# Kernel tuning notes

Hardware: AMD Instinct MI355X
Metric: run time of the kernel (lower is better)

## Reference

```python
import jax, jax.numpy as jnp
import numpy as np

N = 50000   # nodes
E = 800000  # edges (avg degree 16)
D = 128     # feature dim (in_feats and all hidden_feats)
L = 3       # number of SAGEConv layers


def setup_inputs() -> dict:
    key = jax.random.key(0)
    ks = jax.random.split(key, 3 + 3 * L)
    node_feats = jax.random.normal(ks[0], (N, D), dtype=jnp.float32)
    src = jax.random.randint(ks[1], (E,), 0, N)
    dst = jax.random.randint(ks[2], (E,), 0, N)
    inp = {"node_feats": node_feats, "src": src, "dst": dst}
    scale = 1.0 / np.sqrt(D)
    for i in range(L):
        inp[f"W_self{i}"] = (jax.random.normal(ks[3 + 3 * i], (D, D), dtype=jnp.float32) * scale)
        inp[f"W_neigh{i}"] = (jax.random.normal(ks[4 + 3 * i], (D, D), dtype=jnp.float32) * scale)
        inp[f"b{i}"] = jnp.zeros((D,), dtype=jnp.float32)
    return inp


def _sage_stack(node_feats, src, dst, layers):
    n = node_feats.shape[0]
    # in-degree per destination node, clamped so isolated nodes yield 0 aggregate
    deg = jax.ops.segment_sum(jnp.ones((src.shape[0],), dtype=node_feats.dtype), dst, num_segments=n)
    inv_deg = (1.0 / jnp.maximum(deg, 1.0))[:, None]  # [N,1]
    h = node_feats
    for (W_s, W_n, b) in layers:
        # gather neighbor feats along edges, mean-reduce into dst nodes
        agg = jax.ops.segment_sum(h[src], dst, num_segments=n) * inv_deg  # [N,D]
        # DGL SAGEConv ('mean'): fc_self(h_dst) + fc_neigh(mean_neigh) + bias, then activation
        h = jax.nn.relu(h @ W_s.T + agg @ W_n.T + b)
    return h


def reference(node_feats, src, dst, W_self0, W_neigh0, b0, W_self1, W_neigh1, b1, W_self2, W_neigh2, b2):
    layers = ((W_self0, W_neigh0, b0), (W_self1, W_neigh1, b1), (W_self2, W_neigh2, b2))
    return _sage_stack(node_feats, src, dst, layers)
```

## Files before the change

### kernel.cpp

```cpp
#include <hip/hip_runtime.h>
#include <hip/hip_bf16.h>

#define NN 50000
#define NE 800000
#define DF 128
#define NSL 128
#define SLN 391
#define CAP 8192
#define ECHUNK 1563

typedef __bf16 bf16x8 __attribute__((ext_vector_type(8)));
typedef float f32x4 __attribute__((ext_vector_type(4)));

__device__ __forceinline__ unsigned short f32_to_bf16_rne(float f) {
    unsigned int u = __float_as_uint(f);
    u += 0x7fffu + ((u >> 16) & 1u);
    return (unsigned short)(u >> 16);
}

__device__ __forceinline__ unsigned int pack_bf16x2(float lo, float hi) {
    return (unsigned int)f32_to_bf16_rne(lo) | ((unsigned int)f32_to_bf16_rne(hi) << 16);
}

__global__ void k_zero(int* __restrict__ p, int n) {
    int i = threadIdx.x;
    if (i < n) p[i] = 0;
}

__global__ __launch_bounds__(256) void k_bucket(const int* __restrict__ src, const int* __restrict__ dst,
                                                int* __restrict__ gcur, uint2* __restrict__ bucket) {
    __shared__ int cnt[NSL];
    __shared__ int rb[NSL];
    int t = threadIdx.x;
    for (int j = t; j < NSL; j += 256) cnt[j] = 0;
    __syncthreads();
    int base = blockIdx.x * ECHUNK;
    int end = base + ECHUNK;
    if (end > NE) end = NE;
    for (int i = base + t; i < end; i += 256) atomicAdd(&cnt[dst[i] / SLN], 1);
    __syncthreads();
    for (int j = t; j < NSL; j += 256) rb[j] = atomicAdd(&gcur[j], cnt[j]);
    __syncthreads();
    for (int j = t; j < NSL; j += 256) cnt[j] = rb[j];
    __syncthreads();
    for (int i = base + t; i < end; i += 256) {
        int d = dst[i];
        int s = d / SLN;
        int pos = atomicAdd(&cnt[s], 1);
        bucket[s * CAP + pos] = make_uint2((unsigned)src[i], (unsigned)d);
    }
}

__global__ void k_sbase(const int* __restrict__ gcur, int* __restrict__ sbase, int* __restrict__ row_ptr) {
    if (threadIdx.x == 0) {
        int acc = 0;
        for (int s = 0; s < NSL; ++s) {
            sbase[s] = acc;
            acc += gcur[s];
        }
        row_ptr[NN] = acc;
    }
}

__global__ __launch_bounds__(256) void k_cslice(const uint2* __restrict__ bucket, const int* __restrict__ gcur,
                                                const int* __restrict__ sbase, int* __restrict__ col,
                                                int* __restrict__ row_ptr, float* __restrict__ inv_deg) {
    __shared__ int sdeg[512];
    __shared__ int scur[512];
    int s = blockIdx.x;
    int t = threadIdx.x;
    int nbase = s * SLN;
    int ncnt = NN - nbase;
    if (ncnt > SLN) ncnt = SLN;
    int ecnt = gcur[s];
    int eb = s * CAP;
    int cb = sbase[s];
    sdeg[t] = 0;
    sdeg[t + 256] = 0;
    __syncthreads();
    for (int e = t; e < ecnt; e += 256) atomicAdd(&sdeg[bucket[eb + e].y - nbase], 1);
    __syncthreads();
    int d0 = sdeg[t], d1 = sdeg[t + 256];
    for (int off = 1; off < 512; off <<= 1) {
        int v0 = (t >= off) ? sdeg[t - off] : 0;
        int v1 = (t + 256 >= off) ? sdeg[t + 256 - off] : 0;
        __syncthreads();
        sdeg[t] += v0;
        sdeg[t + 256] += v1;
        __syncthreads();
    }
    int e0 = sdeg[t] - d0, e1 = sdeg[t + 256] - d1;
    scur[t] = e0;
    scur[t + 256] = e1;
    if (t < ncnt) {
        row_ptr[nbase + t] = cb + e0;
        inv_deg[nbase + t] = 1.0f / (float)(d0 > 1 ? d0 : 1);
    }
    if (t + 256 < ncnt) {
        row_ptr[nbase + t + 256] = cb + e1;
        inv_deg[nbase + t + 256] = 1.0f / (float)(d1 > 1 ? d1 : 1);
    }
    __syncthreads();
    for (int e = t; e < ecnt; e += 256) {
        uint2 pr = bucket[eb + e];
        int p = atomicAdd(&scur[pr.y - nbase], 1);
        col[cb + p] = (int)pr.x;
    }
}

__global__ __launch_bounds__(256) void k_f2b_all(const float* __restrict__ feats,
                                                 const float* __restrict__ w0, const float* __restrict__ w1,
                                                 const float* __restrict__ w2, const float* __restrict__ w3,
                                                 const float* __restrict__ w4, const float* __restrict__ w5,
                                                 unsigned short* __restrict__ h_bf,
                                                 unsigned short* __restrict__ Wb) {
    int i = (blockIdx.x * 256 + threadIdx.x) * 4;
    const float* fsrc;
    unsigned short* dstp;
    if (i < NN * DF) {
        fsrc = feats + i;
        dstp = h_bf + i;
    } else {
        int j = i - NN * DF;
        if (j >= 6 * DF * DF) return;
        int w = j >> 14;
        int o = j & 16383;
        const float* ws[6] = {w0, w1, w2, w3, w4, w5};
        fsrc = ws[w] + o;
        dstp = Wb + w * DF * DF + o;
    }
    float4 v = *reinterpret_cast<const float4*>(fsrc);
    ushort4 r;
    r.x = f32_to_bf16_rne(v.x);
    r.y = f32_to_bf16_rne(v.y);
    r.z = f32_to_bf16_rne(v.z);
    r.w = f32_to_bf16_rne(v.w);
    *reinterpret_cast<ushort4*>(dstp) = r;
}

__global__ __launch_bounds__(256) void k_agg(const unsigned short* __restrict__ H,
                                             const int* __restrict__ row_ptr, const int* __restrict__ col,
                                             const float* __restrict__ inv_deg,
                                             unsigned short* __restrict__ Agg, int n) {
    int wid = threadIdx.x >> 6;
    int lane = threadIdx.x & 63;
    int node = blockIdx.x * 4 + wid;
    if (node >= n) return;
    int s = row_ptr[node], e = row_ptr[node + 1];
    int g = lane >> 4;
    int l = lane & 15;
    int off = l * 8;

    float a[8];
#pragma unroll
    for (int k = 0; k < 8; ++k) a[k] = 0.f;

    for (int base = s; base < e; base += 64) {
        int rem = e - base;
        if (rem > 64) rem = 64;
        int cl = (lane < rem) ? col[base + lane] : 0;
        for (int jj = 0; jj < rem; jj += 16) {
#pragma unroll
            for (int u = 0; u < 4; ++u) {
                int idx = jj + 4 * u + g;
                int c = __shfl(cl, idx, 64);
                if (idx < rem) {
                    uint4 v = *reinterpret_cast<const uint4*>(H + (size_t)c * DF + off);
                    a[0] += __uint_as_float(v.x << 16);
                    a[1] += __uint_as_float(v.x & 0xffff0000u);
                    a[2] += __uint_as_float(v.y << 16);
                    a[3] += __uint_as_float(v.y & 0xffff0000u);
                    a[4] += __uint_as_float(v.z << 16);
                    a[5] += __uint_as_float(v.z & 0xffff0000u);
                    a[6] += __uint_as_float(v.w << 16);
                    a[7] += __uint_as_float(v.w & 0xffff0000u);
                }
            }
        }
    }

#pragma unroll
    for (int k = 0; k < 8; ++k) {
        a[k] += __shfl_xor(a[k], 16, 64);
        a[k] += __shfl_xor(a[k], 32, 64);
    }

    if (g == 0) {
        float iv = inv_deg[node];
        uint4 r;
        r.x = pack_bf16x2(a[0] * iv, a[1] * iv);
        r.y = pack_bf16x2(a[2] * iv, a[3] * iv);
        r.z = pack_bf16x2(a[4] * iv, a[5] * iv);
        r.w = pack_bf16x2(a[6] * iv, a[7] * iv);
        *reinterpret_cast<uint4*>(Agg + (size_t)node * DF + off) = r;
    }
}

__global__ __launch_bounds__(256) void k_gemm(const unsigned short* __restrict__ Hb,
                                              const unsigned short* __restrict__ Ab,
                                              const unsigned short* __restrict__ Wb,
                                              const float* __restrict__ bias,
                                              unsigned short* __restrict__ Hout,
                                              float* __restrict__ Fout,
                                              int n) {
    int brow = blockIdx.x * 64;
    int lane = threadIdx.x & 63;
    int wid = threadIdx.x >> 6;
    int l15 = lane & 15;
    int lk = (lane >> 4) * 8;
    int colb = wid * 32;

    f32x4 zero = {0.f, 0.f, 0.f, 0.f};
    f32x4 acc[4][2];
#pragma unroll
    for (int m = 0; m < 4; ++m) {
        acc[m][0] = zero;
        acc[m][1] = zero;
    }

#pragma unroll
    for (int ph = 0; ph < 2; ++ph) {
        const unsigned short* Ap = ph ? Ab : Hb;
        const unsigned short* Wp = Wb + ph * (DF * DF);
#pragma unroll
        for (int ks = 0; ks < 4; ++ks) {
            int kb = ks * 32 + lk;
            bf16x8 bfr0 = *reinterpret_cast<const bf16x8*>(Wp + (colb + l15) * DF + kb);
            bf16x8 bfr1 = *reinterpret_cast<const bf16x8*>(Wp + (colb + 16 + l15) * DF + kb);
#pragma unroll
            for (int m = 0; m < 4; ++m) {
                int r = brow + m * 16 + l15;
                if (r >= n) r = n - 1;
                bf16x8 afr = *reinterpret_cast<const bf16x8*>(Ap + (size_t)r * DF + kb);
                acc[m][0] = __builtin_amdgcn_mfma_f32_16x16x32_bf16(afr, bfr0, acc[m][0], 0, 0, 0);
                acc[m][1] = __builtin_amdgcn_mfma_f32_16x16x32_bf16(afr, bfr1, acc[m][1], 0, 0, 0);
            }
        }
    }

    __syncthreads();

    int rb = (lane >> 4) * 4;
#pragma unroll
    for (int q = 0; q < 2; ++q) {
        int o = colb + q * 16 + l15;
        float bv = bias[o];
#pragma unroll
        for (int m = 0; m < 4; ++m) {
#pragma unroll
            for (int j = 0; j < 4; ++j) {
                int r = brow + m * 16 + rb + j;
                if (r < n) {
                    float v = fmaxf(acc[m][q][j] + bv, 0.f);
                    if (Fout) Fout[(size_t)r * DF + o] = v;
                    else Hout[(size_t)r * DF + o] = f32_to_bf16_rne(v);
                }
            }
        }
    }
}

extern "C" void kernel_launch(void* const* d_in, const int* in_sizes, int n_in,
                              void* d_out, int out_size, void* d_ws, size_t ws_size,
                              hipStream_t stream) {
    const float* feats = (const float*)d_in[0];
    const int* src = (const int*)d_in[1];
    const int* dst = (const int*)d_in[2];
    const float* bias[3] = {(const float*)d_in[5], (const float*)d_in[8], (const float*)d_in[11]};

    char* ws = (char*)d_ws;
    unsigned short* h_bf = (unsigned short*)(ws);
    unsigned short* agg_bf = (unsigned short*)(ws + 12800000);
    uint2* bucket = (uint2*)(ws + 12800000);
    unsigned short* Wb = (unsigned short*)(ws + 25600000);
    int* row_ptr = (int*)(ws + 25796608);
    float* inv_deg = (float*)(ws + 25996616);
    int* col = (int*)(ws + 26196616);
    int* gcur = (int*)(ws + 29396616);
    int* sbase = (int*)(ws + 29397128);

    k_zero<<<1, 128, 0, stream>>>(gcur, NSL);
    k_bucket<<<512, 256, 0, stream>>>(src, dst, gcur, bucket);
    k_sbase<<<1, 64, 0, stream>>>(gcur, sbase, row_ptr);
    k_cslice<<<NSL, 256, 0, stream>>>(bucket, gcur, sbase, col, row_ptr, inv_deg);

    int qtot = (NN * DF + 6 * DF * DF) / 4;
    k_f2b_all<<<(qtot + 255) / 256, 256, 0, stream>>>(
        feats, (const float*)d_in[3], (const float*)d_in[4], (const float*)d_in[6],
        (const float*)d_in[7], (const float*)d_in[9], (const float*)d_in[10], h_bf, Wb);

    int gblk = (NN + 63) / 64;
    for (int l = 0; l < 3; ++l) {
        k_agg<<<(NN + 3) / 4, 256, 0, stream>>>(h_bf, row_ptr, col, inv_deg, agg_bf, NN);
        const unsigned short* Wl = Wb + l * 2 * DF * DF;
        if (l < 2)
            k_gemm<<<gblk, 256, 0, stream>>>(h_bf, agg_bf, Wl, bias[l], h_bf, nullptr, NN);
        else
            k_gemm<<<gblk, 256, 0, stream>>>(h_bf, agg_bf, Wl, bias[l], nullptr, (float*)d_out, NN);
    }
}
```

Baseline: 240.0 us.

## Overlap self-GEMM with neighbor aggregation in one interleaved kernel

The self-projection GEMM (h @ W_self + bias) moves into the aggregation kernel as every 17th block, so its MFMA work runs alongside the memory-bound gather. The result is stored as an fp32 temporary that the neighbor GEMM kernel reads back and adds before the ReLU. The separate single-thread prefix-sum kernel is also removed: each k_cslice block now sums the preceding slice counts itself. The cost is an extra fp32 N×D write and read per layer in exchange for one fewer GEMM phase in the critical path.

```diff
diff --git a/kernel.cpp b/kernel.cpp
--- a/kernel.cpp
+++ b/kernel.cpp
@@ -8,6 +8,8 @@
 #define SLN 391
 #define CAP 8192
 #define ECHUNK 1563
+#define GEMMB 782
+#define KA_GRID 13294
 
 typedef __bf16 bf16x8 __attribute__((ext_vector_type(8)));
 typedef float f32x4 __attribute__((ext_vector_type(4)));
@@ -51,22 +53,12 @@
     }
 }
 
-__global__ void k_sbase(const int* __restrict__ gcur, int* __restrict__ sbase, int* __restrict__ row_ptr) {
-    if (threadIdx.x == 0) {
-        int acc = 0;
-        for (int s = 0; s < NSL; ++s) {
-            sbase[s] = acc;
-            acc += gcur[s];
-        }
-        row_ptr[NN] = acc;
-    }
-}
-
 __global__ __launch_bounds__(256) void k_cslice(const uint2* __restrict__ bucket, const int* __restrict__ gcur,
-                                                const int* __restrict__ sbase, int* __restrict__ col,
-                                                int* __restrict__ row_ptr, float* __restrict__ inv_deg) {
+                                                int* __restrict__ col, int* __restrict__ row_ptr,
+                                                float* __restrict__ inv_deg) {
     __shared__ int sdeg[512];
     __shared__ int scur[512];
+    __shared__ int shcb;
     int s = blockIdx.x;
     int t = threadIdx.x;
     int nbase = s * SLN;
@@ -74,10 +66,16 @@
     if (ncnt > SLN) ncnt = SLN;
     int ecnt = gcur[s];
     int eb = s * CAP;
-    int cb = sbase[s];
+    if (t == 0) {
+        int acc = 0;
+        for (int i = 0; i < s; ++i) acc += gcur[i];
+        shcb = acc;
+        if (s == NSL - 1) row_ptr[NN] = acc + ecnt;
+    }
     sdeg[t] = 0;
     sdeg[t + 256] = 0;
     __syncthreads();
+    int cb = shcb;
     for (int e = t; e < ecnt; e += 256) atomicAdd(&sdeg[bucket[eb + e].y - nbase], 1);
     __syncthreads();
     int d0 = sdeg[t], d1 = sdeg[t + 256];
@@ -138,71 +136,121 @@
     *reinterpret_cast<ushort4*>(dstp) = r;
 }
 
-__global__ __launch_bounds__(256) void k_agg(const unsigned short* __restrict__ H,
-                                             const int* __restrict__ row_ptr, const int* __restrict__ col,
-                                             const float* __restrict__ inv_deg,
-                                             unsigned short* __restrict__ Agg, int n) {
+__global__ __launch_bounds__(256) void k_aggself(const unsigned short* __restrict__ H,
+                                                 const int* __restrict__ row_ptr, const int* __restrict__ col,
+                                                 const float* __restrict__ inv_deg,
+                                                 const unsigned short* __restrict__ Ws,
+                                                 const float* __restrict__ bias,
+                                                 unsigned short* __restrict__ Agg,
+                                                 float* __restrict__ Tmp, int n) {
+    int bid = blockIdx.x;
     int wid = threadIdx.x >> 6;
     int lane = threadIdx.x & 63;
-    int node = blockIdx.x * 4 + wid;
-    if (node >= n) return;
-    int s = row_ptr[node], e = row_ptr[node + 1];
     int g = lane >> 4;
     int l = lane & 15;
-    int off = l * 8;
-
-    float a[8];
-#pragma unroll
-    for (int k = 0; k < 8; ++k) a[k] = 0.f;
-
-    for (int base = s; base < e; base += 64) {
-        int rem = e - base;
-        if (rem > 64) rem = 64;
-        int cl = (lane < rem) ? col[base + lane] : 0;
-        for (int jj = 0; jj < rem; jj += 16) {
-#pragma unroll
-            for (int u = 0; u < 4; ++u) {
-                int idx = jj + 4 * u + g;
-                int c = __shfl(cl, idx, 64);
-                if (idx < rem) {
-                    uint4 v = *reinterpret_cast<const uint4*>(H + (size_t)c * DF + off);
-                    a[0] += __uint_as_float(v.x << 16);
-                    a[1] += __uint_as_float(v.x & 0xffff0000u);
-                    a[2] += __uint_as_float(v.y << 16);
-                    a[3] += __uint_as_float(v.y & 0xffff0000u);
-                    a[4] += __uint_as_float(v.z << 16);
-                    a[5] += __uint_as_float(v.z & 0xffff0000u);
-                    a[6] += __uint_as_float(v.w << 16);
-                    a[7] += __uint_as_float(v.w & 0xffff0000u);
+
+    if (bid % 17 != 0) {
+        int agg_id = (bid / 17) * 16 + (bid % 17) - 1;
+        int node = agg_id * 4 + wid;
+        if (node >= n) return;
+        int s = row_ptr[node], e = row_ptr[node + 1];
+        int off = l * 8;
+
+        float a[8];
+#pragma unroll
+        for (int k = 0; k < 8; ++k) a[k] = 0.f;
+
+        for (int base = s; base < e; base += 64) {
+            int rem = e - base;
+            if (rem > 64) rem = 64;
+            int cl = (lane < rem) ? col[base + lane] : 0;
+            for (int jj = 0; jj < rem; jj += 16) {
+#pragma unroll
+                for (int u = 0; u < 4; ++u) {
+                    int idx = jj + 4 * u + g;
+                    int c = __shfl(cl, idx, 64);
+                    if (idx < rem) {
+                        uint4 v = *reinterpret_cast<const uint4*>(H + (size_t)c * DF + off);
+                        a[0] += __uint_as_float(v.x << 16);
+                        a[1] += __uint_as_float(v.x & 0xffff0000u);
+                        a[2] += __uint_as_float(v.y << 16);
+                        a[3] += __uint_as_float(v.y & 0xffff0000u);
+                        a[4] += __uint_as_float(v.z << 16);
+                        a[5] += __uint_as_float(v.z & 0xffff0000u);
+                        a[6] += __uint_as_float(v.w << 16);
+                        a[7] += __uint_as_float(v.w & 0xffff0000u);
+                    }
                 }
             }
         }
-    }
-
-#pragma unroll
-    for (int k = 0; k < 8; ++k) {
-        a[k] += __shfl_xor(a[k], 16, 64);
-        a[k] += __shfl_xor(a[k], 32, 64);
-    }
-
-    if (g == 0) {
-        float iv = inv_deg[node];
-        uint4 r;
-        r.x = pack_bf16x2(a[0] * iv, a[1] * iv);
-        r.y = pack_bf16x2(a[2] * iv, a[3] * iv);
-        r.z = pack_bf16x2(a[4] * iv, a[5] * iv);
-        r.w = pack_bf16x2(a[6] * iv, a[7] * iv);
-        *reinterpret_cast<uint4*>(Agg + (size_t)node * DF + off) = r;
-    }
-}
-
-__global__ __launch_bounds__(256) void k_gemm(const unsigned short* __restrict__ Hb,
-                                              const unsigned short* __restrict__ Ab,
-                                              const unsigned short* __restrict__ Wb,
-                                              const float* __restrict__ bias,
-                                              unsigned short* __restrict__ Hout,
-                                              float* __restrict__ Fout,
-                                              int n) {
+
+#pragma unroll
+        for (int k = 0; k < 8; ++k) {
+            a[k] += __shfl_xor(a[k], 16, 64);
+            a[k] += __shfl_xor(a[k], 32, 64);
+        }
+
+        if (g == 0) {
+            float iv = inv_deg[node];
+            uint4 r;
+            r.x = pack_bf16x2(a[0] * iv, a[1] * iv);
+            r.y = pack_bf16x2(a[2] * iv, a[3] * iv);
+            r.z = pack_bf16x2(a[4] * iv, a[5] * iv);
+            r.w = pack_bf16x2(a[6] * iv, a[7] * iv);
+            *reinterpret_cast<uint4*>(Agg + (size_t)node * DF + off) = r;
+        }
+    } else {
+        int brow = (bid / 17) * 64;
+        int l15 = l;
+        int lk = g * 8;
+        int colb = wid * 32;
+
+        f32x4 zero = {0.f, 0.f, 0.f, 0.f};
+        f32x4 acc[4][2];
+#pragma unroll
+        for (int m = 0; m < 4; ++m) {
+            acc[m][0] = zero;
+            acc[m][1] = zero;
+        }
+
+#pragma unroll
+        for (int ks = 0; ks < 4; ++ks) {
+            int kb = ks * 32 + lk;
+            bf16x8 bfr0 = *reinterpret_cast<const bf16x8*>(Ws + (colb + l15) * DF + kb);
+            bf16x8 bfr1 = *reinterpret_cast<const bf16x8*>(Ws + (colb + 16 + l15) * DF + kb);
+#pragma unroll
+            for (int m = 0; m < 4; ++m) {
+                int r = brow + m * 16 + l15;
+                if (r >= n) r = n - 1;
+                bf16x8 afr = *reinterpret_cast<const bf16x8*>(H + (size_t)r * DF + kb);
+                acc[m][0] = __builtin_amdgcn_mfma_f32_16x16x32_bf16(afr, bfr0, acc[m][0], 0, 0, 0);
+                acc[m][1] = __builtin_amdgcn_mfma_f32_16x16x32_bf16(afr, bfr1, acc[m][1], 0, 0, 0);
+            }
+        }
+
+        int rb = g * 4;
+#pragma unroll
+        for (int q = 0; q < 2; ++q) {
+            int o = colb + q * 16 + l15;
+            float bv = bias[o];
+#pragma unroll
+            for (int m = 0; m < 4; ++m) {
+#pragma unroll
+                for (int j = 0; j < 4; ++j) {
+                    int r = brow + m * 16 + rb + j;
+                    if (r < n) Tmp[(size_t)r * DF + o] = acc[m][q][j] + bv;
+                }
+            }
+        }
+    }
+}
+
+__global__ __launch_bounds__(256) void k_neigh(const unsigned short* __restrict__ Ab,
+                                               const unsigned short* __restrict__ Wn,
+                                               const float* __restrict__ Tmp,
+                                               unsigned short* __restrict__ Hout,
+                                               float* __restrict__ Fout,
+                                               int n) {
     int brow = blockIdx.x * 64;
     int lane = threadIdx.x & 63;
     int wid = threadIdx.x >> 6;
@@ -219,39 +267,31 @@
     }
 
 #pragma unroll
-    for (int ph = 0; ph < 2; ++ph) {
-        const unsigned short* Ap = ph ? Ab : Hb;
-        const unsigned short* Wp = Wb + ph * (DF * DF);
-#pragma unroll
-        for (int ks = 0; ks < 4; ++ks) {
-            int kb = ks * 32 + lk;
-            bf16x8 bfr0 = *reinterpret_cast<const bf16x8*>(Wp + (colb + l15) * DF + kb);
-            bf16x8 bfr1 = *reinterpret_cast<const bf16x8*>(Wp + (colb + 16 + l15) * DF + kb);
-#pragma unroll
-            for (int m = 0; m < 4; ++m) {
-                int r = brow + m * 16 + l15;
-                if (r >= n) r = n - 1;
-                bf16x8 afr = *reinterpret_cast<const bf16x8*>(Ap + (size_t)r * DF + kb);
-                acc[m][0] = __builtin_amdgcn_mfma_f32_16x16x32_bf16(afr, bfr0, acc[m][0], 0, 0, 0);
-                acc[m][1] = __builtin_amdgcn_mfma_f32_16x16x32_bf16(afr, bfr1, acc[m][1], 0, 0, 0);
-            }
-        }
-    }
-
-    __syncthreads();
+    for (int ks = 0; ks < 4; ++ks) {
+        int kb = ks * 32 + lk;
+        bf16x8 bfr0 = *reinterpret_cast<const bf16x8*>(Wn + (colb + l15) * DF + kb);
+        bf16x8 bfr1 = *reinterpret_cast<const bf16x8*>(Wn + (colb + 16 + l15) * DF + kb);
+#pragma unroll
+        for (int m = 0; m < 4; ++m) {
+            int r = brow + m * 16 + l15;
+            if (r >= n) r = n - 1;
+            bf16x8 afr = *reinterpret_cast<const bf16x8*>(Ab + (size_t)r * DF + kb);
+            acc[m][0] = __builtin_amdgcn_mfma_f32_16x16x32_bf16(afr, bfr0, acc[m][0], 0, 0, 0);
+            acc[m][1] = __builtin_amdgcn_mfma_f32_16x16x32_bf16(afr, bfr1, acc[m][1], 0, 0, 0);
+        }
+    }
 
     int rb = (lane >> 4) * 4;
 #pragma unroll
     for (int q = 0; q < 2; ++q) {
         int o = colb + q * 16 + l15;
-        float bv = bias[o];
 #pragma unroll
         for (int m = 0; m < 4; ++m) {
 #pragma unroll
             for (int j = 0; j < 4; ++j) {
                 int r = brow + m * 16 + rb + j;
                 if (r < n) {
-                    float v = fmaxf(acc[m][q][j] + bv, 0.f);
+                    float v = fmaxf(Tmp[(size_t)r * DF + o] + acc[m][q][j], 0.f);
                     if (Fout) Fout[(size_t)r * DF + o] = v;
                     else Hout[(size_t)r * DF + o] = f32_to_bf16_rne(v);
                 }
@@ -277,25 +317,24 @@
     float* inv_deg = (float*)(ws + 25996616);
     int* col = (int*)(ws + 26196616);
     int* gcur = (int*)(ws + 29396616);
-    int* sbase = (int*)(ws + 29397128);
+    float* tmp = (float*)(ws + 29400064);
 
     k_zero<<<1, 128, 0, stream>>>(gcur, NSL);
     k_bucket<<<512, 256, 0, stream>>>(src, dst, gcur, bucket);
-    k_sbase<<<1, 64, 0, stream>>>(gcur, sbase, row_ptr);
-    k_cslice<<<NSL, 256, 0, stream>>>(bucket, gcur, sbase, col, row_ptr, inv_deg);
+    k_cslice<<<NSL, 256, 0, stream>>>(bucket, gcur, col, row_ptr, inv_deg);
 
     int qtot = (NN * DF + 6 * DF * DF) / 4;
     k_f2b_all<<<(qtot + 255) / 256, 256, 0, stream>>>(
         feats, (const float*)d_in[3], (const float*)d_in[4], (const float*)d_in[6],
         (const float*)d_in[7], (const float*)d_in[9], (const float*)d_in[10], h_bf, Wb);
 
-    int gblk = (NN + 63) / 64;
     for (int l = 0; l < 3; ++l) {
-        k_agg<<<(NN + 3) / 4, 256, 0, stream>>>(h_bf, row_ptr, col, inv_deg, agg_bf, NN);
-        const unsigned short* Wl = Wb + l * 2 * DF * DF;
+        const unsigned short* Wsl = Wb + l * 2 * DF * DF;
+        const unsigned short* Wnl = Wsl + DF * DF;
+        k_aggself<<<KA_GRID, 256, 0, stream>>>(h_bf, row_ptr, col, inv_deg, Wsl, bias[l], agg_bf, tmp, NN);
         if (l < 2)
-            k_gemm<<<gblk, 256, 0, stream>>>(h_bf, agg_bf, Wl, bias[l], h_bf, nullptr, NN);
+            k_neigh<<<GEMMB, 256, 0, stream>>>(agg_bf, Wnl, tmp, h_bf, nullptr, NN);
         else
-            k_gemm<<<gblk, 256, 0, stream>>>(h_bf, agg_bf, Wl, bias[l], nullptr, (float*)d_out, NN);
-    }
-}
+            k_neigh<<<GEMMB, 256, 0, stream>>>(agg_bf, Wnl, tmp, nullptr, (float*)d_out, NN);
+    }
+}
```

New measurement: 282.2 us. 17.6% more time.
